# Kernel tuning notes

Hardware: AMD Instinct MI355X
Metric: run time of the kernel (lower is better)

The kernel has to match this reference:

```python
import jax, jax.numpy as jnp
import numpy as np

COST_CLASS, COST_MASK, COST_DICE = 2.0, 5.0, 5.0
NUM_POINTS = 12544

def setup_inputs() -> dict:
    key = jax.random.key(0)
    k1, k2, k3, k4, k5 = jax.random.split(key, 5)
    bs, Q, K = 4, 100, 134
    H = W = 256
    M = 80
    P = H * W
    pred_logits = jax.random.normal(k1, (bs, Q, K), dtype=jnp.float32)
    pred_masks = jax.random.normal(k2, (bs, Q, H, W), dtype=jnp.float32)
    tgt_labels = jax.random.randint(k3, (M,), 0, K - 1, dtype=jnp.int32)
    # binary target masks, stored as float (matches .float() in torch code)
    tgt_masks = (jax.random.uniform(k4, (M, H, W)) > 0.5).astype(jnp.float32)
    # random subset of points without replacement (torch.randperm[:num_points])
    point_idx = jax.random.permutation(k5, P)[:NUM_POINTS].astype(jnp.int32)
    return {"pred_logits": pred_logits, "pred_masks": pred_masks,
            "tgt_labels": tgt_labels, "tgt_masks": tgt_masks,
            "point_idx": point_idx}

def reference(pred_logits, pred_masks, tgt_labels, tgt_masks, point_idx):
    bs, Q, K = pred_logits.shape
    N = bs * Q
    M = tgt_masks.shape[0]
    Pn = point_idx.shape[0]

    # class cost: -p[n, tgt_id[m]]
    out_prob = jax.nn.softmax(pred_logits.reshape(N, K), axis=-1)
    tgt_ids = jnp.clip(tgt_labels.astype(jnp.int32), 0, K - 1)
    cost_class = -out_prob[:, tgt_ids]                      # (N, M)

    # sampled mask logits / targets
    x = pred_masks.reshape(N, -1)[:, point_idx]             # (N, Pn) logits
    y = tgt_masks.reshape(M, -1)[:, point_idx]              # (M, Pn) binary float

    # BCE-with-logits cost, separable form:
    # mean_p[softplus(x) - x*y] = mean_p softplus(x) - (x @ y^T)/Pn
    sp_mean = jnp.mean(jax.nn.softplus(x), axis=-1)         # (N,)
    xy = jnp.einsum('np,mp->nm', x, y)                      # (N, M)
    cost_mask = sp_mean[:, None] - xy / Pn

    # dice cost
    s = jax.nn.sigmoid(x)                                   # (N, Pn)
    numer = 2.0 * jnp.einsum('np,mp->nm', s, y)             # (N, M)
    denom = jnp.sum(s, axis=-1)[:, None] + jnp.sum(y, axis=-1)[None, :]
    cost_dice = 1.0 - (numer + 1.0) / (denom + 1.0)

    C = COST_CLASS * cost_class + COST_MASK * cost_mask + COST_DICE * cost_dice
    return C.reshape(bs, Q, M)
```

## Files before the change

### kernel.cpp

```cpp
#include <hip/hip_runtime.h>
#include <math.h>

#define N_ROWS 400
#define M_ROWS 80
#define K_CLS  134
#define PN     12544
#define PFULL  65536
#define WORDS  (PFULL / 32)
#define NSUB   25
#define KCG    49
#define NM     (N_ROWS * M_ROWS)
#define CHUNK  8192
#define CWORDS (CHUNK / 32)
#define CPB    (PFULL / CHUNK)
#define SPAN   64
#define NIT    8

typedef __attribute__((ext_vector_type(4))) float  f32x4;
typedef __attribute__((ext_vector_type(8))) __bf16 bf16x8;

__device__ __forceinline__ float wave_reduce_sum(float v) {
#pragma unroll
    for (int off = 32; off > 0; off >>= 1) v += __shfl_down(v, off, 64);
    return v;
}

__global__ __launch_bounds__(1024) void sort_softmax_kernel(
        const int* __restrict__ point_idx,
        unsigned int* __restrict__ bitmap_g, int* __restrict__ rank_g,
        int* __restrict__ cw_g,
        float* __restrict__ rowS_acc, float* __restrict__ rowSP_acc,
        float* __restrict__ ysum_acc,
        const float* __restrict__ pred_logits,
        float* __restrict__ rowmax, float* __restrict__ rowsum) {
    int tid = threadIdx.x;
    if (blockIdx.x == 0) {
        __shared__ unsigned int bits[WORDS];
        __shared__ int wtot[16], wbase[16];
        bits[tid] = 0u; bits[tid + 1024] = 0u;
        if (tid < N_ROWS) { rowS_acc[tid] = 0.f; rowSP_acc[tid] = 0.f; }
        if (tid < M_ROWS) ysum_acc[tid] = 0.f;
        __syncthreads();
        for (int i = tid; i < PN; i += 1024) {
            int p = point_idx[i];
            atomicOr(&bits[p >> 5], 1u << (p & 31));
        }
        __syncthreads();
        unsigned int w0 = bits[tid * 2], w1 = bits[tid * 2 + 1];
        int c0 = __popc(w0), c1 = __popc(w1);
        int cnt = c0 + c1;
        int lane = tid & 63, wid = tid >> 6;
        int v = cnt;
#pragma unroll
        for (int off = 1; off < 64; off <<= 1) {
            int u = __shfl_up(v, off, 64);
            if (lane >= off) v += u;
        }
        if (lane == 63) wtot[wid] = v;
        __syncthreads();
        if (tid == 0) {
            int run = 0;
#pragma unroll
            for (int i = 0; i < 16; ++i) { wbase[i] = run; run += wtot[i]; }
        }
        __syncthreads();
        int base = wbase[wid] + (v - cnt);
        bitmap_g[tid * 2]     = w0;
        bitmap_g[tid * 2 + 1] = w1;
        rank_g[tid * 2]       = base;
        rank_g[tid * 2 + 1]   = base + c0;
        {
            int rb = base, c = c0, w = tid * 2;
            int kc = (rb + 255) >> 8;
            if (c > 0 && kc < KCG && kc * 256 < rb + c) cw_g[kc] = w;
        }
        {
            int rb = base + c0, c = c1, w = tid * 2 + 1;
            int kc = (rb + 255) >> 8;
            if (c > 0 && kc < KCG && kc * 256 < rb + c) cw_g[kc] = w;
        }
    } else {
        int wave = tid >> 6, lane = tid & 63;
        int n = (blockIdx.x - 1) * 16 + wave;
        const float* row = pred_logits + n * K_CLS;
        float mx = -1e30f;
        for (int k = lane; k < K_CLS; k += 64) mx = fmaxf(mx, row[k]);
#pragma unroll
        for (int off = 32; off > 0; off >>= 1) mx = fmaxf(mx, __shfl_down(mx, off, 64));
        mx = __shfl(mx, 0, 64);
        float se = 0.f;
        for (int k = lane; k < K_CLS; k += 64) se += expf(row[k] - mx);
        se = wave_reduce_sum(se);
        if (lane == 0) { rowmax[n] = mx; rowsum[n] = se; }
    }
}

__global__ __launch_bounds__(256) void buildY_kernel(
        const float* __restrict__ tgt_masks,
        const unsigned int* __restrict__ bitmap_g, const int* __restrict__ rank_g,
        __bf16* __restrict__ Yc, float* __restrict__ ysum_acc) {
    __shared__ __bf16 comp[CHUNK + 16];
    __shared__ unsigned int sb[CWORDS];
    __shared__ int swb[CWORDS];
    __shared__ float a0[4];
    int b   = blockIdx.x;
    int m = b / CPB, ch = b % CPB;
    int tid = threadIdx.x;
    int wave = tid >> 6, lane = tid & 63;
    int w0  = ch * CWORDS;
    int gb  = rank_g[w0];
    int end = (w0 + CWORDS == WORDS) ? PN : rank_g[w0 + CWORDS];
    int cnt = end - gb;
    sb[tid]  = bitmap_g[w0 + tid];
    swb[tid] = rank_g[w0 + tid] - gb;
    __syncthreads();
    const float* src = tgt_masks + (size_t)m * PFULL + ch * CHUNK;
    int t = CHUNK + (lane & 15);
#pragma unroll
    for (int it = 0; it < CHUNK / (256 * 4); ++it) {
        int e = (it * 256 + tid) * 4;
        f32x4 v = *(const f32x4*)(src + e);
        unsigned int w = sb[e >> 5];
        int bp = e & 31;
        int rb = swb[e >> 5] + __popc(w & ((1u << bp) - 1u));
        unsigned int m4 = (w >> bp) & 0xFu;
        int r0 = (m4 & 1u) ? rb : t;
        int r1 = (m4 & 2u) ? rb + (int)(m4 & 1u) : t;
        int r2 = (m4 & 4u) ? rb + __popc(m4 & 3u) : t;
        int r3 = (m4 & 8u) ? rb + __popc(m4 & 7u) : t;
        comp[r0] = (__bf16)((v[0] > 0.5f) ? 1.f : 0.f);
        comp[r1] = (__bf16)((v[1] > 0.5f) ? 1.f : 0.f);
        comp[r2] = (__bf16)((v[2] > 0.5f) ? 1.f : 0.f);
        comp[r3] = (__bf16)((v[3] > 0.5f) ? 1.f : 0.f);
    }
    __syncthreads();
    __bf16* yrow = Yc + (size_t)m * PN + gb;
    float ys = 0.f;
    for (int i = tid; i < cnt; i += 256) {
        __bf16 y = comp[i];
        yrow[i] = y;
        ys += (float)y;
    }
    ys = wave_reduce_sum(ys);
    if (lane == 0) a0[wave] = ys;
    __syncthreads();
    if (tid == 0)
        atomicAdd(&ysum_acc[m], a0[0] + a0[1] + a0[2] + a0[3]);
}

__global__ __launch_bounds__(256) void gemm_fused_kernel(
        const float* __restrict__ pred_masks,
        const __bf16* __restrict__ Yc,
        const unsigned int* __restrict__ bitmap_g,
        const int* __restrict__ rank_g, const int* __restrict__ cw_g,
        float* __restrict__ xypart, float* __restrict__ sypart,
        float* __restrict__ rowS_acc, float* __restrict__ rowSP_acc) {
    __shared__ __align__(16) unsigned char smem[20992];
    __bf16* comp      = (__bf16*)smem;
    unsigned int* sw  = (unsigned int*)(smem + 8704);
    int* sr           = (int*)(smem + 8960);
    float (*red)[20][64] = (float (*)[20][64])smem;
    float (*rowred)[2][16] = (float (*)[2][16])(smem + 20480);

    int tid = threadIdx.x;
    int wave = tid >> 6, lane = tid & 63;
    int colL = lane & 15, quad = lane >> 4;
    int nsub = blockIdx.x % NSUB, kcg = blockIdx.x / NSUB;
    int n0 = nsub * 16;
    int wlo = cw_g[kcg];
    int ew  = (kcg == KCG - 1) ? (WORDS - 1) : cw_g[kcg + 1];
    int S = ew - wlo + 1; if (S > SPAN) S = SPAN;
    int E4 = S * 8;
    int rbase = kcg * 256;
    for (int i = tid; i < S; i += 256) {
        sw[i] = bitmap_g[wlo + i];
        sr[i] = rank_g[wlo + i] - rbase;
    }
    bf16x8 Bb[2][5];
#pragma unroll
    for (int i = 0; i < 2; ++i) {
        int k0 = kcg * 256 + (wave * 2 + i) * 32 + quad * 8;
#pragma unroll
        for (int j = 0; j < 5; ++j)
            Bb[i][j] = *(const bf16x8*)(Yc + (size_t)(16 * j + colL) * PN + k0);
    }
    __syncthreads();

    int trash = 256 + (lane & 15);
#pragma unroll 1
    for (int rp = 0; rp < 2; ++rp) {
        int rowA = wave + rp * 8;
        int rowB = rowA + 4;
        const float* srcA = pred_masks + (size_t)(n0 + rowA) * PFULL + (size_t)wlo * 32;
        const float* srcB = pred_masks + (size_t)(n0 + rowB) * PFULL + (size_t)wlo * 32;
        __bf16* crowA = comp + rowA * 272;
        __bf16* crowB = comp + rowB * 272;
        f32x4 va[NIT], vb2[NIT];
#pragma unroll
        for (int it = 0; it < NIT; ++it) {
            int e4 = lane + it * 64;
            int e4c = (e4 < E4) ? e4 : (E4 - 1);
            va[it]  = *(const f32x4*)(srcA + (size_t)e4c * 4);
            vb2[it] = *(const f32x4*)(srcB + (size_t)e4c * 4);
        }
        __builtin_amdgcn_sched_barrier(0);
#pragma unroll
        for (int it = 0; it < NIT; ++it) {
            int e4 = lane + it * 64;
            int e4c = (e4 < E4) ? e4 : (E4 - 1);
            unsigned int w = sw[e4c >> 3];
            int bp = (e4c & 7) * 4;
            int rb = sr[e4c >> 3] + __popc(w & ((1u << bp) - 1u));
            unsigned int m4 = (w >> bp) & 0xFu;
            int r0 = rb;
            int r1 = rb + (int)(m4 & 1u);
            int r2 = rb + __popc(m4 & 3u);
            int r3 = rb + __popc(m4 & 7u);
            r0 = ((m4 & 1u) && (unsigned)r0 < 256u) ? r0 : trash;
            r1 = ((m4 & 2u) && (unsigned)r1 < 256u) ? r1 : trash;
            r2 = ((m4 & 4u) && (unsigned)r2 < 256u) ? r2 : trash;
            r3 = ((m4 & 8u) && (unsigned)r3 < 256u) ? r3 : trash;
            crowA[r0] = (__bf16)va[it][0];
            crowA[r1] = (__bf16)va[it][1];
            crowA[r2] = (__bf16)va[it][2];
            crowA[r3] = (__bf16)va[it][3];
            crowB[r0] = (__bf16)vb2[it][0];
            crowB[r1] = (__bf16)vb2[it][1];
            crowB[r2] = (__bf16)vb2[it][2];
            crowB[r3] = (__bf16)vb2[it][3];
        }
    }
    __syncthreads();

    f32x4 accX[5], accS[5];
    f32x4 zero = {0.f, 0.f, 0.f, 0.f};
#pragma unroll
    for (int j = 0; j < 5; ++j) { accX[j] = zero; accS[j] = zero; }
    float sS = 0.f, sSP = 0.f;
#pragma unroll
    for (int i = 0; i < 2; ++i) {
        int kl = (wave * 2 + i) * 32 + quad * 8;
        bf16x8 aX = *(const bf16x8*)&comp[colL * 272 + kl];
        bf16x8 aSg;
#pragma unroll
        for (int jj = 0; jj < 8; ++jj) {
            float x  = (float)aX[jj];
            float ax = fabsf(x);
            float ee = __expf(-ax);
            float den = 1.f + ee;
            float inv = __builtin_amdgcn_rcpf(den);
            float sig = (x >= 0.f) ? inv : ee * inv;
            float sp  = fmaxf(x, 0.f) + __logf(den);
            aSg[jj] = (__bf16)sig;
            sS += sig; sSP += sp;
        }
#pragma unroll
        for (int j = 0; j < 5; ++j) {
            accX[j] = __builtin_amdgcn_mfma_f32_16x16x32_bf16(aX,  Bb[i][j], accX[j], 0, 0, 0);
            accS[j] = __builtin_amdgcn_mfma_f32_16x16x32_bf16(aSg, Bb[i][j], accS[j], 0, 0, 0);
        }
    }
    sS  += __shfl_down(sS, 32, 64);
    sS  += __shfl_down(sS, 16, 64);
    sSP += __shfl_down(sSP, 32, 64);
    sSP += __shfl_down(sSP, 16, 64);
    if (lane < 16) { rowred[wave][0][lane] = sS; rowred[wave][1][lane] = sSP; }
    __syncthreads();

#pragma unroll
    for (int j = 0; j < 5; ++j)
#pragma unroll
        for (int r = 0; r < 4; ++r) red[wave][j * 4 + r][lane] = accX[j][r];
    __syncthreads();
#pragma unroll
    for (int v0 = 0; v0 < 5; ++v0) {
        int v = wave * 5 + v0;
        float s = red[0][v][lane] + red[1][v][lane] + red[2][v][lane] + red[3][v][lane];
        int j = v >> 2, r = v & 3;
        int n = n0 + quad * 4 + r, m = 16 * j + colL;
        xypart[(size_t)kcg * NM + n * M_ROWS + m] = s;
    }
    if (tid < 16) {
        atomicAdd(&rowS_acc[n0 + tid],
                  rowred[0][0][tid] + rowred[1][0][tid] +
                  rowred[2][0][tid] + rowred[3][0][tid]);
    } else if (tid < 32) {
        int l = tid - 16;
        atomicAdd(&rowSP_acc[n0 + l],
                  rowred[0][1][l] + rowred[1][1][l] +
                  rowred[2][1][l] + rowred[3][1][l]);
    }
    __syncthreads();
#pragma unroll
    for (int j = 0; j < 5; ++j)
#pragma unroll
        for (int r = 0; r < 4; ++r) red[wave][j * 4 + r][lane] = accS[j][r];
    __syncthreads();
#pragma unroll
    for (int v0 = 0; v0 < 5; ++v0) {
        int v = wave * 5 + v0;
        float s = red[0][v][lane] + red[1][v][lane] + red[2][v][lane] + red[3][v][lane];
        int j = v >> 2, r = v & 3;
        int n = n0 + quad * 4 + r, m = 16 * j + colL;
        sypart[(size_t)kcg * NM + n * M_ROWS + m] = s;
    }
}

__global__ __launch_bounds__(256) void combine_kernel(
        const float* __restrict__ logits,
        const int* __restrict__ tgt_labels,
        const float* __restrict__ rowmax,
        const float* __restrict__ rowsum,
        const float* __restrict__ rowS_acc,
        const float* __restrict__ rowSP_acc,
        const float* __restrict__ ysum_acc,
        const float* __restrict__ xypart,
        const float* __restrict__ sypart,
        float* __restrict__ out) {
    __shared__ float sxy[4][64], ssy[4][64];
    int il = threadIdx.x & 63, q = threadIdx.x >> 6;
    int idx = blockIdx.x * 64 + il;
    int n = idx / M_ROWS, m = idx % M_ROWS;
    float xy = 0.f, sy = 0.f;
    for (int g = q; g < KCG; g += 4) {
        xy += xypart[(size_t)g * NM + idx];
        sy += sypart[(size_t)g * NM + idx];
    }
    sxy[q][il] = xy; ssy[q][il] = sy;
    __syncthreads();
    if (q == 0) {
        xy = sxy[0][il] + sxy[1][il] + sxy[2][il] + sxy[3][il];
        sy = ssy[0][il] + ssy[1][il] + ssy[2][il] + ssy[3][il];
        float ss = rowS_acc[n], sp = rowSP_acc[n], ysum = ysum_acc[m];
        int tc = tgt_labels[m];
        tc = min(max(tc, 0), K_CLS - 1);
        float p = expf(logits[n * K_CLS + tc] - rowmax[n]) / rowsum[n];
        float cost_class = -p;
        float cost_mask = (sp - xy) * (1.0f / PN);
        float cost_dice = 1.f - (2.f * sy + 1.f) / (ss + ysum + 1.f);
        out[idx] = 2.f * cost_class + 5.f * cost_mask + 5.f * cost_dice;
    }
}

extern "C" void kernel_launch(void* const* d_in, const int* in_sizes, int n_in,
                              void* d_out, int out_size, void* d_ws, size_t ws_size,
                              hipStream_t stream) {
    const float* pred_logits = (const float*)d_in[0];
    const float* pred_masks  = (const float*)d_in[1];
    const int*   tgt_labels  = (const int*)d_in[2];
    const float* tgt_masks   = (const float*)d_in[3];
    const int*   point_idx   = (const int*)d_in[4];
    float* out = (float*)d_out;

    char* ws = (char*)d_ws;
    size_t off = 0;
    auto carve = [&](size_t nbytes) {
        char* p = ws + off;
        off += (nbytes + 255) & ~(size_t)255;
        return p;
    };
    unsigned int* bitmap = (unsigned int*)carve(WORDS * 4);
    int*   rankp  = (int*)carve(WORDS * 4);
    int*   cw     = (int*)carve(KCG * 4);
    float* rowmax = (float*)carve(N_ROWS * 4);
    float* rowsum = (float*)carve(N_ROWS * 4);
    float* rowS_acc  = (float*)carve(N_ROWS * 4);
    float* rowSP_acc = (float*)carve(N_ROWS * 4);
    float* ysum_acc  = (float*)carve(M_ROWS * 4);
    __bf16* Yc = (__bf16*)carve((size_t)M_ROWS * PN * 2);
    float* xypart = (float*)carve((size_t)KCG * NM * 4);
    float* sypart = (float*)carve((size_t)KCG * NM * 4);
    (void)ws_size; (void)in_sizes; (void)n_in; (void)out_size;

    sort_softmax_kernel<<<26, 1024, 0, stream>>>(
        point_idx, bitmap, rankp, cw, rowS_acc, rowSP_acc, ysum_acc,
        pred_logits, rowmax, rowsum);
    buildY_kernel<<<M_ROWS * CPB, 256, 0, stream>>>(
        tgt_masks, bitmap, rankp, Yc, ysum_acc);
    gemm_fused_kernel<<<NSUB * KCG, 256, 0, stream>>>(
        pred_masks, Yc, bitmap, rankp, cw, xypart, sypart,
        rowS_acc, rowSP_acc);
    combine_kernel<<<NM / 64, 256, 0, stream>>>(
        pred_logits, tgt_labels, rowmax, rowsum, rowS_acc, rowSP_acc,
        ysum_acc, xypart, sypart, out);
}
```

Before: 203.5 us.

## Double gemm_fused block to 512 threads with one row pair per wave

```diff
diff --git a/kernel.cpp b/kernel.cpp
--- a/kernel.cpp
+++ b/kernel.cpp
@@ -148,19 +148,19 @@
         atomicAdd(&ysum_acc[m], a0[0] + a0[1] + a0[2] + a0[3]);
 }
 
-__global__ __launch_bounds__(256) void gemm_fused_kernel(
+__global__ __launch_bounds__(512, 2) void gemm_fused_kernel(
         const float* __restrict__ pred_masks,
         const __bf16* __restrict__ Yc,
         const unsigned int* __restrict__ bitmap_g,
         const int* __restrict__ rank_g, const int* __restrict__ cw_g,
         float* __restrict__ xypart, float* __restrict__ sypart,
         float* __restrict__ rowS_acc, float* __restrict__ rowSP_acc) {
-    __shared__ __align__(16) unsigned char smem[20992];
+    __shared__ __align__(16) unsigned char smem[41984];
     __bf16* comp      = (__bf16*)smem;
     unsigned int* sw  = (unsigned int*)(smem + 8704);
     int* sr           = (int*)(smem + 8960);
     float (*red)[20][64] = (float (*)[20][64])smem;
-    float (*rowred)[2][16] = (float (*)[2][16])(smem + 20480);
+    float (*rowred)[2][16] = (float (*)[2][16])(smem + 40960);
 
     int tid = threadIdx.x;
     int wave = tid >> 6, lane = tid & 63;
@@ -172,25 +172,22 @@
     int S = ew - wlo + 1; if (S > SPAN) S = SPAN;
     int E4 = S * 8;
     int rbase = kcg * 256;
-    for (int i = tid; i < S; i += 256) {
+    for (int i = tid; i < S; i += 512) {
         sw[i] = bitmap_g[wlo + i];
         sr[i] = rank_g[wlo + i] - rbase;
     }
-    bf16x8 Bb[2][5];
-#pragma unroll
-    for (int i = 0; i < 2; ++i) {
-        int k0 = kcg * 256 + (wave * 2 + i) * 32 + quad * 8;
+    bf16x8 Bb[5];
+    {
+        int k0 = rbase + wave * 32 + quad * 8;
 #pragma unroll
         for (int j = 0; j < 5; ++j)
-            Bb[i][j] = *(const bf16x8*)(Yc + (size_t)(16 * j + colL) * PN + k0);
+            Bb[j] = *(const bf16x8*)(Yc + (size_t)(16 * j + colL) * PN + k0);
     }
     __syncthreads();
 
     int trash = 256 + (lane & 15);
-#pragma unroll 1
-    for (int rp = 0; rp < 2; ++rp) {
-        int rowA = wave + rp * 8;
-        int rowB = rowA + 4;
+    {
+        int rowA = wave, rowB = wave + 8;
         const float* srcA = pred_masks + (size_t)(n0 + rowA) * PFULL + (size_t)wlo * 32;
         const float* srcB = pred_masks + (size_t)(n0 + rowB) * PFULL + (size_t)wlo * 32;
         __bf16* crowA = comp + rowA * 272;
@@ -237,9 +234,8 @@
 #pragma unroll
     for (int j = 0; j < 5; ++j) { accX[j] = zero; accS[j] = zero; }
     float sS = 0.f, sSP = 0.f;
-#pragma unroll
-    for (int i = 0; i < 2; ++i) {
-        int kl = (wave * 2 + i) * 32 + quad * 8;
+    {
+        int kl = wave * 32 + quad * 8;
         bf16x8 aX = *(const bf16x8*)&comp[colL * 272 + kl];
         bf16x8 aSg;
 #pragma unroll
@@ -256,8 +252,8 @@
         }
 #pragma unroll
         for (int j = 0; j < 5; ++j) {
-            accX[j] = __builtin_amdgcn_mfma_f32_16x16x32_bf16(aX,  Bb[i][j], accX[j], 0, 0, 0);
-            accS[j] = __builtin_amdgcn_mfma_f32_16x16x32_bf16(aSg, Bb[i][j], accS[j], 0, 0, 0);
+            accX[j] = __builtin_amdgcn_mfma_f32_16x16x32_bf16(aX,  Bb[j], accX[j], 0, 0, 0);
+            accS[j] = __builtin_amdgcn_mfma_f32_16x16x32_bf16(aSg, Bb[j], accS[j], 0, 0, 0);
         }
     }
     sS  += __shfl_down(sS, 32, 64);
@@ -272,23 +268,24 @@
 #pragma unroll
         for (int r = 0; r < 4; ++r) red[wave][j * 4 + r][lane] = accX[j][r];
     __syncthreads();
-#pragma unroll
-    for (int v0 = 0; v0 < 5; ++v0) {
-        int v = wave * 5 + v0;
-        float s = red[0][v][lane] + red[1][v][lane] + red[2][v][lane] + red[3][v][lane];
+    for (int v = wave; v < 20; v += 8) {
+        float s = red[0][v][lane] + red[1][v][lane] + red[2][v][lane] + red[3][v][lane]
+                + red[4][v][lane] + red[5][v][lane] + red[6][v][lane] + red[7][v][lane];
         int j = v >> 2, r = v & 3;
         int n = n0 + quad * 4 + r, m = 16 * j + colL;
         xypart[(size_t)kcg * NM + n * M_ROWS + m] = s;
     }
     if (tid < 16) {
-        atomicAdd(&rowS_acc[n0 + tid],
-                  rowred[0][0][tid] + rowred[1][0][tid] +
-                  rowred[2][0][tid] + rowred[3][0][tid]);
+        float s = 0.f;
+#pragma unroll
+        for (int w = 0; w < 8; ++w) s += rowred[w][0][tid];
+        atomicAdd(&rowS_acc[n0 + tid], s);
     } else if (tid < 32) {
         int l = tid - 16;
-        atomicAdd(&rowSP_acc[n0 + l],
-                  rowred[0][1][l] + rowred[1][1][l] +
-                  rowred[2][1][l] + rowred[3][1][l]);
+        float s = 0.f;
+#pragma unroll
+        for (int w = 0; w < 8; ++w) s += rowred[w][1][l];
+        atomicAdd(&rowSP_acc[n0 + l], s);
     }
     __syncthreads();
 #pragma unroll
@@ -296,10 +293,9 @@
 #pragma unroll
         for (int r = 0; r < 4; ++r) red[wave][j * 4 + r][lane] = accS[j][r];
     __syncthreads();
-#pragma unroll
-    for (int v0 = 0; v0 < 5; ++v0) {
-        int v = wave * 5 + v0;
-        float s = red[0][v][lane] + red[1][v][lane] + red[2][v][lane] + red[3][v][lane];
+    for (int v = wave; v < 20; v += 8) {
+        float s = red[0][v][lane] + red[1][v][lane] + red[2][v][lane] + red[3][v][lane]
+                + red[4][v][lane] + red[5][v][lane] + red[6][v][lane] + red[7][v][lane];
         int j = v >> 2, r = v & 3;
         int n = n0 + quad * 4 + r, m = 16 * j + colL;
         sypart[(size_t)kcg * NM + n * M_ROWS + m] = s;
@@ -377,7 +373,7 @@
         pred_logits, rowmax, rowsum);
     buildY_kernel<<<M_ROWS * CPB, 256, 0, stream>>>(
         tgt_masks, bitmap, rankp, Yc, ysum_acc);
-    gemm_fused_kernel<<<NSUB * KCG, 256, 0, stream>>>(
+    gemm_fused_kernel<<<NSUB * KCG, 512, 0, stream>>>(
         pred_masks, Yc, bitmap, rankp, cw, xypart, sypart,
         rowS_acc, rowSP_acc);
     combine_kernel<<<NM / 64, 256, 0, stream>>>(
```

New measurement: 202.6 us. No clear change (-0.4%).
